# Kernel tuning notes

Measured on AMD Instinct MI355X. Metric: run time of the kernel, lower is better.

Reference implementation:

```python
import jax, jax.numpy as jnp
import numpy as np

K = 8
LN_EPS = 1e-5


def setup_inputs() -> dict:
    key = jax.random.key(0)
    ks = jax.random.split(key, 12)
    Nq, N, d = 2048, 50000, 256
    xav = np.sqrt(6.0 / (d + d)).astype(np.float32)
    inp = {
        "query": jax.random.normal(ks[0], (Nq, d), jnp.float32),
        "query_pos": jax.random.uniform(ks[1], (Nq, 3), jnp.float32) * 10.0,
        "inst_feats": jax.random.normal(ks[2], (N, d), jnp.float32),
        "sp_coords": jax.random.uniform(ks[3], (N, 3), jnp.float32) * 10.0,
        "w_q": jax.random.uniform(ks[4], (d, d), jnp.float32, -xav, xav),
        "w_v": jax.random.uniform(ks[5], (d, d), jnp.float32, -xav, xav),
        "w_o": jax.random.uniform(ks[6], (d, d), jnp.float32, -xav, xav),
        # original inits w_k/w_b to zero (uniform gate); use small random for a nontrivial gate
        "w_k": jax.random.normal(ks[7], (K, d), jnp.float32) * 0.02,
        "w_b": jax.random.normal(ks[8], (K,), jnp.float32) * 0.02,
        "gamma": jnp.ones((d,), jnp.float32),
        "beta": jnp.zeros((d,), jnp.float32),
    }
    return inp


def _knn_idx(query_pos, sp_coords, k):
    # squared euclidean distances [Nq, N] via ||q||^2 - 2 q.p + ||p||^2
    d2 = (
        jnp.sum(query_pos * query_pos, -1, keepdims=True)
        - 2.0 * (query_pos @ sp_coords.T)
        + jnp.sum(sp_coords * sp_coords, -1)[None, :]
    )
    _, idx = jax.lax.top_k(-d2, k)  # [Nq, k] nearest-neighbor indices
    return idx


def reference(query, query_pos, inst_feats, sp_coords, w_q, w_v, w_o, w_k, w_b, gamma, beta):
    idx = _knn_idx(query_pos, sp_coords, K)
    feat = inst_feats[idx]                       # [Nq, k, d] gathered neighbor feats
    q = query @ w_q.T                            # [Nq, d]
    v = feat @ w_v.T                             # [Nq, k, d]
    gate = jax.nn.softmax(q @ w_k.T + w_b, -1)   # [Nq, k]
    w = jnp.einsum("qk,qkd->qd", gate, q[:, None, :] * v)
    out = w @ w_o.T + query                      # dropout p=0 -> identity; residual
    mu = jnp.mean(out, -1, keepdims=True)
    var = jnp.mean((out - mu) ** 2, -1, keepdims=True)
    return (out - mu) * jax.lax.rsqrt(var + LN_EPS) * gamma + beta
```

## Files before the change

### kernel.cpp

```cpp
#include <hip/hip_runtime.h>
#include <math.h>

#define D        256
#define KNN      8
#define G        16
#define NCELL    (G*G*G)
#define CS       0.625f
#define EPS_D2   2e-3f
#define CAP      64
#define SPILLMAX 50000

typedef unsigned long long u64;
typedef __attribute__((ext_vector_type(8))) short bf16x8;
typedef __attribute__((ext_vector_type(4))) float f32x4;

__device__ __forceinline__ unsigned short f2b(float f) {
    unsigned u = __float_as_uint(f);
    u += 0x7fff + ((u >> 16) & 1);
    return (unsigned short)(u >> 16);
}
__device__ __forceinline__ bf16x8 pack8(float4 a, float4 b) {
    bf16x8 r;
    r[0] = (short)f2b(a.x); r[1] = (short)f2b(a.y);
    r[2] = (short)f2b(a.z); r[3] = (short)f2b(a.w);
    r[4] = (short)f2b(b.x); r[5] = (short)f2b(b.y);
    r[6] = (short)f2b(b.z); r[7] = (short)f2b(b.w);
    return r;
}

__device__ __forceinline__ unsigned enc_f32(float f) {
    unsigned b = __float_as_uint(f);
    return b ^ ((unsigned)(((int)b) >> 31) | 0x80000000u);
}
__device__ __forceinline__ float dec_f32(unsigned t) {
    unsigned m = (unsigned)(((int)t) >> 31);
    return __uint_as_float(t ^ (0x80000000u | ~m));
}
__device__ __forceinline__ u64 mkkey(float d2, int j) {
    return ((u64)enc_f32(d2) << 32) | (u64)(unsigned)j;
}
__device__ __forceinline__ int cell_of(float x) {
    int c = (int)(x * 1.6f);
    return c < 0 ? 0 : (c > G-1 ? G-1 : c);
}

__global__ __launch_bounds__(256) void prep(const float* __restrict__ w_k,
                                            const float* __restrict__ w_q,
                                            const float* __restrict__ w_v,
                                            const float* __restrict__ w_o,
                                            float* __restrict__ wk2,
                                            unsigned short* __restrict__ wqb,
                                            unsigned short* __restrict__ wvb,
                                            unsigned short* __restrict__ wob,
                                            int4* __restrict__ cnt4,
                                            int* __restrict__ spill_cnt)
{
    const int b = blockIdx.x, t = threadIdx.x;
    if (b < 8) {
        float acc = 0.f;
#pragma unroll 8
        for (int d = 0; d < D; ++d)
            acc = fmaf(w_k[b*D + d], w_q[(size_t)d*D + t], acc);
        wk2[b*D + t] = acc;
    } else if (b < 12) {
        cnt4[(b-8)*256 + t] = make_int4(0, 0, 0, 0);
        if (b == 8 && t == 0) *spill_cnt = 0;
    } else {
        const int m = (b - 12) >> 5;
        const int local = (b - 12) & 31;
        const size_t e = (size_t)local * 2048 + (size_t)t * 8;
        const float* src = (m == 0) ? w_q : (m == 1) ? w_v : w_o;
        unsigned short* dst = (m == 0) ? wqb : (m == 1) ? wvb : wob;
        const float4 x0 = *(const float4*)&src[e];
        const float4 x1 = *(const float4*)&src[e + 4];
        *(bf16x8*)&dst[e] = pack8(x0, x1);
    }
}

__global__ __launch_bounds__(256) void scatter_bins(const float* __restrict__ spc,
                                                    int* __restrict__ cnt,
                                                    float4* __restrict__ bins,
                                                    int* __restrict__ spill_cnt,
                                                    float4* __restrict__ spill, int N)
{
    const int j = blockIdx.x * 256 + threadIdx.x;
    if (j >= N) return;
    const float px = spc[3*j+0], py = spc[3*j+1], pz = spc[3*j+2];
    const int cell = cell_of(px) | (cell_of(py) << 4) | (cell_of(pz) << 8);
    const float4 p = make_float4(px, py, pz, __int_as_float(j));
    const int pos = atomicAdd(&cnt[cell], 1);
    if (pos < CAP) bins[cell*CAP + pos] = p;
    else {
        const int sp = atomicAdd(spill_cnt, 1);
        if (sp < SPILLMAX) spill[sp] = p;
    }
}

#define INSERT8(xk)                                                            \
    if ((xk) < k7) {                                                           \
        const bool c0 = (xk) < k0, c1 = (xk) < k1, c2 = (xk) < k2,             \
                   c3 = (xk) < k3, c4 = (xk) < k4, c5 = (xk) < k5,             \
                   c6 = (xk) < k6;                                             \
        k7 = c6 ? k6 : (xk);                                                   \
        k6 = c5 ? k5 : (c6 ? (xk) : k6);                                       \
        k5 = c4 ? k4 : (c5 ? (xk) : k5);                                       \
        k4 = c3 ? k3 : (c4 ? (xk) : k4);                                       \
        k3 = c2 ? k2 : (c3 ? (xk) : k3);                                       \
        k2 = c1 ? k1 : (c2 ? (xk) : k2);                                       \
        k1 = c0 ? k0 : (c1 ? (xk) : k1);                                       \
        k0 = c0 ? (xk) : k0;                                                   \
    }

#define SCORE(p)                                                               \
    {                                                                          \
        const float sp  = __fadd_rn(__fadd_rn(__fmul_rn((p).x,(p).x),          \
                                  __fmul_rn((p).y,(p).y)), __fmul_rn((p).z,(p).z)); \
        const float dot = __fmaf_rn(qz,(p).z, __fmaf_rn(qy,(p).y, __fmul_rn(qx,(p).x))); \
        const float d2  = __fadd_rn(__fsub_rn(sq, __fmul_rn(2.0f, dot)), sp);  \
        const u64 xk = mkkey(d2, __float_as_int((p).w));                       \
        INSERT8(xk)                                                            \
    }

__device__ __forceinline__ void wave_merge8(int l, u64& k0, u64& k1, u64& k2, u64& k3,
                                            u64& k4, u64& k5, u64& k6, u64& k7,
                                            u64& mine)
{
#pragma unroll
    for (int rd = 0; rd < KNN; ++rd) {
        u64 m = k0;
#pragma unroll
        for (int o = 32; o; o >>= 1) {
            const u64 t = __shfl_xor(m, o);
            if (t < m) m = t;
        }
        if (k0 == m) {
            k0 = k1; k1 = k2; k2 = k3; k3 = k4; k4 = k5; k5 = k6; k6 = k7;
            k7 = ~0ull;
        }
        if (l == rd) mine = m;
    }
}

__global__ __launch_bounds__(512) void mega2(const float* __restrict__ qpos,
                                             const float4* __restrict__ bins,
                                             const int* __restrict__ cnt,
                                             const int* __restrict__ spill_cnt,
                                             const float4* __restrict__ spill,
                                             const float* __restrict__ query,
                                             const float* __restrict__ wk2,
                                             const float* __restrict__ w_b,
                                             const float* __restrict__ feats,
                                             const unsigned short* __restrict__ wqb,
                                             const unsigned short* __restrict__ wvb,
                                             const unsigned short* __restrict__ wob,
                                             const float* __restrict__ gmm,
                                             const float* __restrict__ bta,
                                             float* __restrict__ out)
{
    __shared__ unsigned short a_lds[16][264];
    __shared__ unsigned short f_lds[16][264];
    __shared__ unsigned short w_lds[16][264];
    __shared__ float q_f32[8][260];
    __shared__ float o_f32[8][260];

    const int tid = threadIdx.x;
    const int wv  = tid >> 6, l = tid & 63;
    const int r0  = blockIdx.x * 8;

    {
        const int arr = tid >> 8;
        const int row = 8 + ((tid >> 5) & 7);
        const int o8  = (tid & 31) * 8;
        const bf16x8 z = {0,0,0,0,0,0,0,0};
        if (arr == 0) *(bf16x8*)&a_lds[row][o8] = z;
        else          *(bf16x8*)&f_lds[row][o8] = z;
    }

    {
        const int q = r0 + wv;
        const float qx = qpos[3*q+0], qy = qpos[3*q+1], qz = qpos[3*q+2];
        const float sq = __fadd_rn(__fadd_rn(__fmul_rn(qx,qx), __fmul_rn(qy,qy)),
                                   __fmul_rn(qz,qz));
        const int cx = cell_of(qx), cy = cell_of(qy), cz = cell_of(qz);

        auto bstart = [](int c, float coord) {
            const float f = coord * 1.6f - (float)c;
            int b = c + ((f < 0.5f) ? -2 : -1);
            return b < 0 ? 0 : (b > G-4 ? G-4 : b);
        };
        const int bx = bstart(cx, qx), by = bstart(cy, qy), bz = bstart(cz, qz);

        u64 k0 = ~0ull, k1 = ~0ull, k2 = ~0ull, k3 = ~0ull,
            k4 = ~0ull, k5 = ~0ull, k6 = ~0ull, k7 = ~0ull;

        {
            const int x = bx + (l & 3), y = by + ((l >> 2) & 3), z = bz + (l >> 4);
            const int ci = x | (y << 4) | (z << 8);
            const int n = min(cnt[ci], CAP);
            const int st = ci * CAP;
            for (int i = 0; i < n; ++i) { const float4 p = bins[st + i]; SCORE(p) }
        }
        {
            const int ns = min(*spill_cnt, SPILLMAX);
            for (int i = l; i < ns; i += 64) { const float4 p = spill[i]; SCORE(p) }
        }

        u64 mine = ~0ull;
        wave_merge8(l, k0, k1, k2, k3, k4, k5, k6, k7, mine);
        const u64 worst = __shfl(mine, KNN-1);

        const float w8 = dec_f32((unsigned)(worst >> 32));
        float dmin = INFINITY;
        if (bx > 0)     dmin = fminf(dmin, qx - (float)bx * CS);
        if (bx + 4 < G) dmin = fminf(dmin, (float)(bx + 4) * CS - qx);
        if (by > 0)     dmin = fminf(dmin, qy - (float)by * CS);
        if (by + 4 < G) dmin = fminf(dmin, (float)(by + 4) * CS - qy);
        if (bz > 0)     dmin = fminf(dmin, qz - (float)bz * CS);
        if (bz + 4 < G) dmin = fminf(dmin, (float)(bz + 4) * CS - qz);

        if (!(w8 + EPS_D2 <= dmin * dmin)) {
            k0 = (l < KNN) ? mine : ~0ull;
            k1 = ~0ull; k2 = ~0ull; k3 = ~0ull; k4 = ~0ull;
            k5 = ~0ull; k6 = ~0ull; k7 = ~0ull;
            for (int c = l; c < NCELL; c += 64) {
                const int x = c & 15, y = (c >> 4) & 15, z = c >> 8;
                if (x >= bx && x < bx+4 && y >= by && y < by+4 && z >= bz && z < bz+4) continue;
                const int n = min(cnt[c], CAP);
                const int st = c * CAP;
                for (int i = 0; i < n; ++i) { const float4 p = bins[st + i]; SCORE(p) }
            }
            wave_merge8(l, k0, k1, k2, k3, k4, k5, k6, k7, mine);
        }

        int ids[KNN];
        const int my_id = (int)(unsigned)(mine & 0xffffffffu);
#pragma unroll
        for (int j = 0; j < KNN; ++j) ids[j] = __shfl(my_id, j);

        const float4 qv = *(const float4*)&query[(size_t)q*D + l*4];
        float logit[KNN];
#pragma unroll
        for (int j = 0; j < KNN; ++j) {
            const float4 w = *(const float4*)&wk2[(size_t)j*D + l*4];
            logit[j] = fmaf(qv.x, w.x, fmaf(qv.y, w.y, fmaf(qv.z, w.z, qv.w*w.w)));
        }
#pragma unroll
        for (int o = 32; o; o >>= 1) {
#pragma unroll
            for (int j = 0; j < KNN; ++j) logit[j] += __shfl_xor(logit[j], o);
        }
#pragma unroll
        for (int j = 0; j < KNN; ++j) logit[j] += w_b[j];

        float m = logit[0];
#pragma unroll
        for (int j = 1; j < KNN; ++j) m = fmaxf(m, logit[j]);
        float e[KNN]; float ssum = 0.f;
#pragma unroll
        for (int j = 0; j < KNN; ++j) { e[j] = expf(logit[j] - m); ssum += e[j]; }
        const float inv = 1.f / ssum;

        float4 acc4 = make_float4(0.f, 0.f, 0.f, 0.f);
#pragma unroll
        for (int j = 0; j < KNN; ++j) {
            const float gj = e[j] * inv;
            const float4 f = *(const float4*)&feats[(size_t)ids[j]*D + l*4];
            acc4.x = fmaf(gj, f.x, acc4.x);
            acc4.y = fmaf(gj, f.y, acc4.y);
            acc4.z = fmaf(gj, f.z, acc4.z);
            acc4.w = fmaf(gj, f.w, acc4.w);
        }

        *(float4*)&q_f32[wv][l*4] = qv;
        short4 qb; qb.x = (short)f2b(qv.x); qb.y = (short)f2b(qv.y);
                   qb.z = (short)f2b(qv.z); qb.w = (short)f2b(qv.w);
        *(short4*)&a_lds[wv][l*4] = qb;
        short4 fb; fb.x = (short)f2b(acc4.x); fb.y = (short)f2b(acc4.y);
                   fb.z = (short)f2b(acc4.z); fb.w = (short)f2b(acc4.w);
        *(short4*)&f_lds[wv][l*4] = fb;
    }
    __syncthreads();

    const int mrow = l & 15;
    const int kq   = (l >> 4) * 8;

    f32x4 aq[2], av[2];
#pragma unroll
    for (int t = 0; t < 2; ++t) {
        aq[t] = (f32x4){0.f, 0.f, 0.f, 0.f};
        av[t] = (f32x4){0.f, 0.f, 0.f, 0.f};
    }
#pragma unroll
    for (int k0 = 0; k0 < D; k0 += 32) {
        const bf16x8 af = *(const bf16x8*)&a_lds[mrow][k0 + kq];
        const bf16x8 ff = *(const bf16x8*)&f_lds[mrow][k0 + kq];
#pragma unroll
        for (int t = 0; t < 2; ++t) {
            const int n = wv*32 + t*16 + mrow;
            const bf16x8 bq = *(const bf16x8*)&wqb[(size_t)n*D + k0 + kq];
            const bf16x8 bv = *(const bf16x8*)&wvb[(size_t)n*D + k0 + kq];
            aq[t] = __builtin_amdgcn_mfma_f32_16x16x32_bf16(af, bq, aq[t], 0, 0, 0);
            av[t] = __builtin_amdgcn_mfma_f32_16x16x32_bf16(ff, bv, av[t], 0, 0, 0);
        }
    }

#pragma unroll
    for (int t = 0; t < 2; ++t) {
#pragma unroll
        for (int r = 0; r < 4; ++r) {
            const int row = (l >> 4) * 4 + r;
            const int col = wv*32 + t*16 + (l & 15);
            w_lds[row][col] = f2b(aq[t][r] * av[t][r]);
        }
    }
    __syncthreads();

    f32x4 ao[2];
#pragma unroll
    for (int t = 0; t < 2; ++t) ao[t] = (f32x4){0.f, 0.f, 0.f, 0.f};
#pragma unroll
    for (int k0 = 0; k0 < D; k0 += 32) {
        const bf16x8 wf = *(const bf16x8*)&w_lds[mrow][k0 + kq];
#pragma unroll
        for (int t = 0; t < 2; ++t) {
            const int n = wv*32 + t*16 + mrow;
            const bf16x8 bo = *(const bf16x8*)&wob[(size_t)n*D + k0 + kq];
            ao[t] = __builtin_amdgcn_mfma_f32_16x16x32_bf16(wf, bo, ao[t], 0, 0, 0);
        }
    }
#pragma unroll
    for (int t = 0; t < 2; ++t) {
#pragma unroll
        for (int r = 0; r < 4; ++r) {
            const int row = (l >> 4) * 4 + r;
            if (row < 8) {
                const int col = wv*32 + t*16 + (l & 15);
                o_f32[row][col] = ao[t][r] + q_f32[row][col];
            }
        }
    }
    __syncthreads();

    {
        const float4 v = *(const float4*)&o_f32[wv][l*4];
        float s  = (v.x + v.y) + (v.z + v.w);
        float s2 = fmaf(v.x, v.x, fmaf(v.y, v.y, fmaf(v.z, v.z, v.w*v.w)));
#pragma unroll
        for (int o = 32; o; o >>= 1) { s += __shfl_xor(s, o); s2 += __shfl_xor(s2, o); }
        const float mu  = s * (1.f/256.f);
        const float var = fmaf(s2, 1.f/256.f, -mu*mu);
        const float rs  = rsqrtf(var + 1e-5f);
        const float4 g = *(const float4*)&gmm[l*4];
        const float4 b = *(const float4*)&bta[l*4];
        float4 o4;
        o4.x = (v.x - mu) * rs * g.x + b.x;
        o4.y = (v.y - mu) * rs * g.y + b.y;
        o4.z = (v.z - mu) * rs * g.z + b.z;
        o4.w = (v.w - mu) * rs * g.w + b.w;
        *(float4*)&out[(size_t)(r0+wv)*D + l*4] = o4;
    }
}

extern "C" void kernel_launch(void* const* d_in, const int* in_sizes, int n_in,
                              void* d_out, int out_size, void* d_ws, size_t ws_size,
                              hipStream_t stream)
{
    const float* query = (const float*)d_in[0];
    const float* qpos  = (const float*)d_in[1];
    const float* feats = (const float*)d_in[2];
    const float* spc   = (const float*)d_in[3];
    const float* w_q   = (const float*)d_in[4];
    const float* w_v   = (const float*)d_in[5];
    const float* w_o   = (const float*)d_in[6];
    const float* w_k   = (const float*)d_in[7];
    const float* w_b   = (const float*)d_in[8];
    const float* gamma = (const float*)d_in[9];
    const float* beta  = (const float*)d_in[10];

    const int Nq = in_sizes[0] / D;
    const int N  = in_sizes[2] / D;

    char* ws = (char*)d_ws;
    size_t off = 0;
    int* cnt = (int*)(ws + off);               off += ((size_t)NCELL * 4 + 255) & ~(size_t)255;
    int* spill_cnt = (int*)(ws + off);         off += 256;
    float* wk2 = (float*)(ws + off);           off += ((size_t)KNN * D * 4 + 255) & ~(size_t)255;
    unsigned short* wqb = (unsigned short*)(ws + off); off += (size_t)D * D * 2;
    unsigned short* wvb = (unsigned short*)(ws + off); off += (size_t)D * D * 2;
    unsigned short* wob = (unsigned short*)(ws + off); off += (size_t)D * D * 2;
    float4* bins = (float4*)(ws + off);        off += ((size_t)NCELL * CAP * 16 + 255) & ~(size_t)255;
    float4* spill = (float4*)(ws + off);       off += ((size_t)SPILLMAX * 16 + 255) & ~(size_t)255;

    prep<<<108, 256, 0, stream>>>(w_k, w_q, w_v, w_o, wk2, wqb, wvb, wob,
                                  (int4*)cnt, spill_cnt);
    scatter_bins<<<(N + 255)/256, 256, 0, stream>>>(spc, cnt, bins, spill_cnt, spill, N);
    mega2<<<Nq/8, 512, 0, stream>>>(qpos, bins, cnt, spill_cnt, spill,
                                    query, wk2, w_b, feats, wqb, wvb, wob,
                                    gamma, beta, (float*)d_out);
}
```

Baseline: 52.81 us.

## Fuse prep, binning and attention into one cooperative persistent kernel

Replaces the three launches (weight prep, spatial binning scatter, main kNN+MLP kernel) with a single cooperative kernel of 512 blocks that uses grid-wide syncs between phases, then loops persistently over 4-query tiles. The per-block tile shrinks from 8 to 4 queries with 256 threads, each wave covering 64 output columns. This removes kernel launch gaps at the cost of grid.sync overhead and a persistent loop that reloads the weight fragments per tile. The old three-kernel path remains as a fallback if the cooperative launch fails.

```diff
diff --git a/kernel.cpp b/kernel.cpp
--- a/kernel.cpp
+++ b/kernel.cpp
@@ -1,5 +1,8 @@
 #include <hip/hip_runtime.h>
+#include <hip/hip_cooperative_groups.h>
 #include <math.h>
+
+namespace cg = cooperative_groups;
 
 #define D        256
 #define KNN      8
@@ -9,6 +12,7 @@
 #define EPS_D2   2e-3f
 #define CAP      64
 #define SPILLMAX 50000
+#define GRIDC    512
 
 typedef unsigned long long u64;
 typedef __attribute__((ext_vector_type(8))) short bf16x8;
@@ -42,6 +46,332 @@
 __device__ __forceinline__ int cell_of(float x) {
     int c = (int)(x * 1.6f);
     return c < 0 ? 0 : (c > G-1 ? G-1 : c);
+}
+
+#define INSERT8(xk)                                                            \
+    if ((xk) < k7) {                                                           \
+        const bool c0 = (xk) < k0, c1 = (xk) < k1, c2 = (xk) < k2,             \
+                   c3 = (xk) < k3, c4 = (xk) < k4, c5 = (xk) < k5,             \
+                   c6 = (xk) < k6;                                             \
+        k7 = c6 ? k6 : (xk);                                                   \
+        k6 = c5 ? k5 : (c6 ? (xk) : k6);                                       \
+        k5 = c4 ? k4 : (c5 ? (xk) : k5);                                       \
+        k4 = c3 ? k3 : (c4 ? (xk) : k4);                                       \
+        k3 = c2 ? k2 : (c3 ? (xk) : k3);                                       \
+        k2 = c1 ? k1 : (c2 ? (xk) : k2);                                       \
+        k1 = c0 ? k0 : (c1 ? (xk) : k1);                                       \
+        k0 = c0 ? (xk) : k0;                                                   \
+    }
+
+#define SCORE(p)                                                               \
+    {                                                                          \
+        const float sp  = __fadd_rn(__fadd_rn(__fmul_rn((p).x,(p).x),          \
+                                  __fmul_rn((p).y,(p).y)), __fmul_rn((p).z,(p).z)); \
+        const float dot = __fmaf_rn(qz,(p).z, __fmaf_rn(qy,(p).y, __fmul_rn(qx,(p).x))); \
+        const float d2  = __fadd_rn(__fsub_rn(sq, __fmul_rn(2.0f, dot)), sp);  \
+        const u64 xk = mkkey(d2, __float_as_int((p).w));                       \
+        INSERT8(xk)                                                            \
+    }
+
+__device__ __forceinline__ void wave_merge8(int l, u64& k0, u64& k1, u64& k2, u64& k3,
+                                            u64& k4, u64& k5, u64& k6, u64& k7,
+                                            u64& mine)
+{
+#pragma unroll
+    for (int rd = 0; rd < KNN; ++rd) {
+        u64 m = k0;
+#pragma unroll
+        for (int o = 32; o; o >>= 1) {
+            const u64 t = __shfl_xor(m, o);
+            if (t < m) m = t;
+        }
+        if (k0 == m) {
+            k0 = k1; k1 = k2; k2 = k3; k3 = k4; k4 = k5; k5 = k6; k6 = k7;
+            k7 = ~0ull;
+        }
+        if (l == rd) mine = m;
+    }
+}
+
+__device__ __forceinline__ void knn_gate_wave(int q, int l,
+                                              const float* __restrict__ qpos,
+                                              const float4* __restrict__ bins,
+                                              const int* __restrict__ cnt,
+                                              const int* __restrict__ spill_cnt,
+                                              const float4* __restrict__ spill,
+                                              const float* __restrict__ query,
+                                              const float* __restrict__ wk2,
+                                              const float* __restrict__ w_b,
+                                              const float* __restrict__ feats,
+                                              float4& qv_out, float4& fb_out)
+{
+    const float qx = qpos[3*q+0], qy = qpos[3*q+1], qz = qpos[3*q+2];
+    const float sq = __fadd_rn(__fadd_rn(__fmul_rn(qx,qx), __fmul_rn(qy,qy)),
+                               __fmul_rn(qz,qz));
+    const int cx = cell_of(qx), cy = cell_of(qy), cz = cell_of(qz);
+
+    auto bstart = [](int c, float coord) {
+        const float f = coord * 1.6f - (float)c;
+        int b = c + ((f < 0.5f) ? -2 : -1);
+        return b < 0 ? 0 : (b > G-4 ? G-4 : b);
+    };
+    const int bx = bstart(cx, qx), by = bstart(cy, qy), bz = bstart(cz, qz);
+
+    u64 k0 = ~0ull, k1 = ~0ull, k2 = ~0ull, k3 = ~0ull,
+        k4 = ~0ull, k5 = ~0ull, k6 = ~0ull, k7 = ~0ull;
+
+    {
+        const int x = bx + (l & 3), y = by + ((l >> 2) & 3), z = bz + (l >> 4);
+        const int ci = x | (y << 4) | (z << 8);
+        const int n = min(cnt[ci], CAP);
+        const int st = ci * CAP;
+        for (int i = 0; i < n; ++i) { const float4 p = bins[st + i]; SCORE(p) }
+    }
+    {
+        const int ns = min(*spill_cnt, SPILLMAX);
+        for (int i = l; i < ns; i += 64) { const float4 p = spill[i]; SCORE(p) }
+    }
+
+    u64 mine = ~0ull;
+    wave_merge8(l, k0, k1, k2, k3, k4, k5, k6, k7, mine);
+    const u64 worst = __shfl(mine, KNN-1);
+
+    const float w8 = dec_f32((unsigned)(worst >> 32));
+    float dmin = INFINITY;
+    if (bx > 0)     dmin = fminf(dmin, qx - (float)bx * CS);
+    if (bx + 4 < G) dmin = fminf(dmin, (float)(bx + 4) * CS - qx);
+    if (by > 0)     dmin = fminf(dmin, qy - (float)by * CS);
+    if (by + 4 < G) dmin = fminf(dmin, (float)(by + 4) * CS - qy);
+    if (bz > 0)     dmin = fminf(dmin, qz - (float)bz * CS);
+    if (bz + 4 < G) dmin = fminf(dmin, (float)(bz + 4) * CS - qz);
+
+    if (!(w8 + EPS_D2 <= dmin * dmin)) {
+        k0 = (l < KNN) ? mine : ~0ull;
+        k1 = ~0ull; k2 = ~0ull; k3 = ~0ull; k4 = ~0ull;
+        k5 = ~0ull; k6 = ~0ull; k7 = ~0ull;
+        for (int c = l; c < NCELL; c += 64) {
+            const int x = c & 15, y = (c >> 4) & 15, z = c >> 8;
+            if (x >= bx && x < bx+4 && y >= by && y < by+4 && z >= bz && z < bz+4) continue;
+            const int n = min(cnt[c], CAP);
+            const int st = c * CAP;
+            for (int i = 0; i < n; ++i) { const float4 p = bins[st + i]; SCORE(p) }
+        }
+        wave_merge8(l, k0, k1, k2, k3, k4, k5, k6, k7, mine);
+    }
+
+    int ids[KNN];
+    const int my_id = (int)(unsigned)(mine & 0xffffffffu);
+#pragma unroll
+    for (int j = 0; j < KNN; ++j) ids[j] = __shfl(my_id, j);
+
+    const float4 qv = *(const float4*)&query[(size_t)q*D + l*4];
+    float logit[KNN];
+#pragma unroll
+    for (int j = 0; j < KNN; ++j) {
+        const float4 w = *(const float4*)&wk2[(size_t)j*D + l*4];
+        logit[j] = fmaf(qv.x, w.x, fmaf(qv.y, w.y, fmaf(qv.z, w.z, qv.w*w.w)));
+    }
+#pragma unroll
+    for (int o = 32; o; o >>= 1) {
+#pragma unroll
+        for (int j = 0; j < KNN; ++j) logit[j] += __shfl_xor(logit[j], o);
+    }
+#pragma unroll
+    for (int j = 0; j < KNN; ++j) logit[j] += w_b[j];
+
+    float m = logit[0];
+#pragma unroll
+    for (int j = 1; j < KNN; ++j) m = fmaxf(m, logit[j]);
+    float e[KNN]; float ssum = 0.f;
+#pragma unroll
+    for (int j = 0; j < KNN; ++j) { e[j] = expf(logit[j] - m); ssum += e[j]; }
+    const float inv = 1.f / ssum;
+
+    float4 acc4 = make_float4(0.f, 0.f, 0.f, 0.f);
+#pragma unroll
+    for (int j = 0; j < KNN; ++j) {
+        const float gj = e[j] * inv;
+        const float4 f = *(const float4*)&feats[(size_t)ids[j]*D + l*4];
+        acc4.x = fmaf(gj, f.x, acc4.x);
+        acc4.y = fmaf(gj, f.y, acc4.y);
+        acc4.z = fmaf(gj, f.z, acc4.z);
+        acc4.w = fmaf(gj, f.w, acc4.w);
+    }
+    qv_out = qv;
+    fb_out = acc4;
+}
+
+struct MegaParams {
+    const float* qpos; const float* spc; const float* query; const float* feats;
+    const float* w_k; const float* w_q; const float* w_v; const float* w_o;
+    const float* w_b; const float* gmm; const float* bta;
+    float* wk2;
+    unsigned short* wqb; unsigned short* wvb; unsigned short* wob;
+    int* cnt; int* spill_cnt; float4* bins; float4* spill;
+    float* out;
+    int N; int Nq;
+};
+
+__global__ __launch_bounds__(256, 2) void megacoop(MegaParams P)
+{
+    __shared__ unsigned short a_lds[16][264];
+    __shared__ unsigned short f_lds[16][264];
+    __shared__ unsigned short w_lds[16][264];
+    __shared__ float q_f32[4][260];
+    __shared__ float o_f32[4][260];
+
+    cg::grid_group gg = cg::this_grid();
+    const int tid = threadIdx.x;
+    const int g   = blockIdx.x * 256 + tid;
+    const int wv  = tid >> 6, l = tid & 63;
+
+    if (g < 16384) {
+        const int o = g >> 3, sub = g & 7;
+        const int row = o >> 8, col = o & 255;
+        float acc = 0.f;
+#pragma unroll 8
+        for (int i = 0; i < 32; ++i) {
+            const int d = sub * 32 + i;
+            acc = fmaf(P.w_k[row*D + d], P.w_q[(size_t)d*D + col], acc);
+        }
+        acc += __shfl_xor(acc, 1);
+        acc += __shfl_xor(acc, 2);
+        acc += __shfl_xor(acc, 4);
+        if (sub == 0) P.wk2[o] = acc;
+    } else if (g < 17408) {
+        ((int4*)P.cnt)[g - 16384] = make_int4(0, 0, 0, 0);
+        if (g == 16384) *P.spill_cnt = 0;
+    } else if (g < 41984) {
+        const int o = g - 17408;
+        const int m = o >> 13, local = o & 8191;
+        const size_t e = (size_t)local * 8;
+        const float* src = (m == 0) ? P.w_q : (m == 1) ? P.w_v : P.w_o;
+        unsigned short* dst = (m == 0) ? P.wqb : (m == 1) ? P.wvb : P.wob;
+        const float4 x0 = *(const float4*)&src[e];
+        const float4 x1 = *(const float4*)&src[e + 4];
+        *(bf16x8*)&dst[e] = pack8(x0, x1);
+    }
+    gg.sync();
+
+    if (g < P.N) {
+        const int j = g;
+        const float px = P.spc[3*j+0], py = P.spc[3*j+1], pz = P.spc[3*j+2];
+        const int cell = cell_of(px) | (cell_of(py) << 4) | (cell_of(pz) << 8);
+        const float4 p = make_float4(px, py, pz, __int_as_float(j));
+        const int pos = atomicAdd(&P.cnt[cell], 1);
+        if (pos < CAP) P.bins[cell*CAP + pos] = p;
+        else {
+            const int sp = atomicAdd(P.spill_cnt, 1);
+            if (sp < SPILLMAX) P.spill[sp] = p;
+        }
+    }
+    gg.sync();
+
+    for (int t0 = blockIdx.x * 4; t0 < P.Nq; t0 += GRIDC * 4) {
+#pragma unroll
+        for (int k = 0; k < 3; ++k) {
+            const int o = tid + k * 256;
+            const int oo = (o < 384) ? o : o - 384;
+            const int row = 4 + (oo >> 5);
+            const int c8 = (oo & 31) * 8;
+            const bf16x8 z = {0,0,0,0,0,0,0,0};
+            if (o < 384) *(bf16x8*)&a_lds[row][c8] = z;
+            else         *(bf16x8*)&f_lds[row][c8] = z;
+        }
+
+        {
+            float4 qv, fb;
+            knn_gate_wave(t0 + wv, l, P.qpos, P.bins, P.cnt, P.spill_cnt, P.spill,
+                          P.query, P.wk2, P.w_b, P.feats, qv, fb);
+            *(float4*)&q_f32[wv][l*4] = qv;
+            short4 qb; qb.x = (short)f2b(qv.x); qb.y = (short)f2b(qv.y);
+                       qb.z = (short)f2b(qv.z); qb.w = (short)f2b(qv.w);
+            *(short4*)&a_lds[wv][l*4] = qb;
+            short4 fv; fv.x = (short)f2b(fb.x); fv.y = (short)f2b(fb.y);
+                       fv.z = (short)f2b(fb.z); fv.w = (short)f2b(fb.w);
+            *(short4*)&f_lds[wv][l*4] = fv;
+        }
+        __syncthreads();
+
+        const int mrow = l & 15;
+        const int kq   = (l >> 4) * 8;
+
+        f32x4 aq[4], av[4];
+#pragma unroll
+        for (int t = 0; t < 4; ++t) {
+            aq[t] = (f32x4){0.f, 0.f, 0.f, 0.f};
+            av[t] = (f32x4){0.f, 0.f, 0.f, 0.f};
+        }
+#pragma unroll
+        for (int k0 = 0; k0 < D; k0 += 32) {
+            const bf16x8 af = *(const bf16x8*)&a_lds[mrow][k0 + kq];
+            const bf16x8 ff = *(const bf16x8*)&f_lds[mrow][k0 + kq];
+#pragma unroll
+            for (int t = 0; t < 4; ++t) {
+                const int n = wv*64 + t*16 + mrow;
+                const bf16x8 bq = *(const bf16x8*)&P.wqb[(size_t)n*D + k0 + kq];
+                const bf16x8 bv = *(const bf16x8*)&P.wvb[(size_t)n*D + k0 + kq];
+                aq[t] = __builtin_amdgcn_mfma_f32_16x16x32_bf16(af, bq, aq[t], 0, 0, 0);
+                av[t] = __builtin_amdgcn_mfma_f32_16x16x32_bf16(ff, bv, av[t], 0, 0, 0);
+            }
+        }
+#pragma unroll
+        for (int t = 0; t < 4; ++t) {
+#pragma unroll
+            for (int r = 0; r < 4; ++r) {
+                const int row = (l >> 4) * 4 + r;
+                const int col = wv*64 + t*16 + (l & 15);
+                w_lds[row][col] = f2b(aq[t][r] * av[t][r]);
+            }
+        }
+        __syncthreads();
+
+        f32x4 ao[4];
+#pragma unroll
+        for (int t = 0; t < 4; ++t) ao[t] = (f32x4){0.f, 0.f, 0.f, 0.f};
+#pragma unroll
+        for (int k0 = 0; k0 < D; k0 += 32) {
+            const bf16x8 wf = *(const bf16x8*)&w_lds[mrow][k0 + kq];
+#pragma unroll
+            for (int t = 0; t < 4; ++t) {
+                const int n = wv*64 + t*16 + mrow;
+                const bf16x8 bo = *(const bf16x8*)&P.wob[(size_t)n*D + k0 + kq];
+                ao[t] = __builtin_amdgcn_mfma_f32_16x16x32_bf16(wf, bo, ao[t], 0, 0, 0);
+            }
+        }
+#pragma unroll
+        for (int t = 0; t < 4; ++t) {
+#pragma unroll
+            for (int r = 0; r < 4; ++r) {
+                const int row = (l >> 4) * 4 + r;
+                if (row < 4) {
+                    const int col = wv*64 + t*16 + (l & 15);
+                    o_f32[row][col] = ao[t][r] + q_f32[row][col];
+                }
+            }
+        }
+        __syncthreads();
+
+        {
+            const float4 v = *(const float4*)&o_f32[wv][l*4];
+            float s  = (v.x + v.y) + (v.z + v.w);
+            float s2 = fmaf(v.x, v.x, fmaf(v.y, v.y, fmaf(v.z, v.z, v.w*v.w)));
+#pragma unroll
+            for (int o = 32; o; o >>= 1) { s += __shfl_xor(s, o); s2 += __shfl_xor(s2, o); }
+            const float mu  = s * (1.f/256.f);
+            const float var = fmaf(s2, 1.f/256.f, -mu*mu);
+            const float rs  = rsqrtf(var + 1e-5f);
+            const float4 gm = *(const float4*)&P.gmm[l*4];
+            const float4 bt = *(const float4*)&P.bta[l*4];
+            float4 o4;
+            o4.x = (v.x - mu) * rs * gm.x + bt.x;
+            o4.y = (v.y - mu) * rs * gm.y + bt.y;
+            o4.z = (v.z - mu) * rs * gm.z + bt.z;
+            o4.w = (v.w - mu) * rs * gm.w + bt.w;
+            *(float4*)&P.out[(size_t)(t0+wv)*D + l*4] = o4;
+        }
+        __syncthreads();
+    }
 }
 
 __global__ __launch_bounds__(256) void prep(const float* __restrict__ w_k,
@@ -96,51 +426,6 @@
     }
 }
 
-#define INSERT8(xk)                                                            \
-    if ((xk) < k7) {                                                           \
-        const bool c0 = (xk) < k0, c1 = (xk) < k1, c2 = (xk) < k2,             \
-                   c3 = (xk) < k3, c4 = (xk) < k4, c5 = (xk) < k5,             \
-                   c6 = (xk) < k6;                                             \
-        k7 = c6 ? k6 : (xk);                                                   \
-        k6 = c5 ? k5 : (c6 ? (xk) : k6);                                       \
-        k5 = c4 ? k4 : (c5 ? (xk) : k5);                                       \
-        k4 = c3 ? k3 : (c4 ? (xk) : k4);                                       \
-        k3 = c2 ? k2 : (c3 ? (xk) : k3);                                       \
-        k2 = c1 ? k1 : (c2 ? (xk) : k2);                                       \
-        k1 = c0 ? k0 : (c1 ? (xk) : k1);                                       \
-        k0 = c0 ? (xk) : k0;                                                   \
-    }
-
-#define SCORE(p)                                                               \
-    {                                                                          \
-        const float sp  = __fadd_rn(__fadd_rn(__fmul_rn((p).x,(p).x),          \
-                                  __fmul_rn((p).y,(p).y)), __fmul_rn((p).z,(p).z)); \
-        const float dot = __fmaf_rn(qz,(p).z, __fmaf_rn(qy,(p).y, __fmul_rn(qx,(p).x))); \
-        const float d2  = __fadd_rn(__fsub_rn(sq, __fmul_rn(2.0f, dot)), sp);  \
-        const u64 xk = mkkey(d2, __float_as_int((p).w));                       \
-        INSERT8(xk)                                                            \
-    }
-
-__device__ __forceinline__ void wave_merge8(int l, u64& k0, u64& k1, u64& k2, u64& k3,
-                                            u64& k4, u64& k5, u64& k6, u64& k7,
-                                            u64& mine)
-{
-#pragma unroll
-    for (int rd = 0; rd < KNN; ++rd) {
-        u64 m = k0;
-#pragma unroll
-        for (int o = 32; o; o >>= 1) {
-            const u64 t = __shfl_xor(m, o);
-            if (t < m) m = t;
-        }
-        if (k0 == m) {
-            k0 = k1; k1 = k2; k2 = k3; k3 = k4; k4 = k5; k5 = k6; k6 = k7;
-            k7 = ~0ull;
-        }
-        if (l == rd) mine = m;
-    }
-}
-
 __global__ __launch_bounds__(512) void mega2(const float* __restrict__ qpos,
                                              const float4* __restrict__ bins,
                                              const int* __restrict__ cnt,
@@ -177,107 +462,16 @@
     }
 
     {
-        const int q = r0 + wv;
-        const float qx = qpos[3*q+0], qy = qpos[3*q+1], qz = qpos[3*q+2];
-        const float sq = __fadd_rn(__fadd_rn(__fmul_rn(qx,qx), __fmul_rn(qy,qy)),
-                                   __fmul_rn(qz,qz));
-        const int cx = cell_of(qx), cy = cell_of(qy), cz = cell_of(qz);
-
-        auto bstart = [](int c, float coord) {
-            const float f = coord * 1.6f - (float)c;
-            int b = c + ((f < 0.5f) ? -2 : -1);
-            return b < 0 ? 0 : (b > G-4 ? G-4 : b);
-        };
-        const int bx = bstart(cx, qx), by = bstart(cy, qy), bz = bstart(cz, qz);
-
-        u64 k0 = ~0ull, k1 = ~0ull, k2 = ~0ull, k3 = ~0ull,
-            k4 = ~0ull, k5 = ~0ull, k6 = ~0ull, k7 = ~0ull;
-
-        {
-            const int x = bx + (l & 3), y = by + ((l >> 2) & 3), z = bz + (l >> 4);
-            const int ci = x | (y << 4) | (z << 8);
-            const int n = min(cnt[ci], CAP);
-            const int st = ci * CAP;
-            for (int i = 0; i < n; ++i) { const float4 p = bins[st + i]; SCORE(p) }
-        }
-        {
-            const int ns = min(*spill_cnt, SPILLMAX);
-            for (int i = l; i < ns; i += 64) { const float4 p = spill[i]; SCORE(p) }
-        }
-
-        u64 mine = ~0ull;
-        wave_merge8(l, k0, k1, k2, k3, k4, k5, k6, k7, mine);
-        const u64 worst = __shfl(mine, KNN-1);
-
-        const float w8 = dec_f32((unsigned)(worst >> 32));
-        float dmin = INFINITY;
-        if (bx > 0)     dmin = fminf(dmin, qx - (float)bx * CS);
-        if (bx + 4 < G) dmin = fminf(dmin, (float)(bx + 4) * CS - qx);
-        if (by > 0)     dmin = fminf(dmin, qy - (float)by * CS);
-        if (by + 4 < G) dmin = fminf(dmin, (float)(by + 4) * CS - qy);
-        if (bz > 0)     dmin = fminf(dmin, qz - (float)bz * CS);
-        if (bz + 4 < G) dmin = fminf(dmin, (float)(bz + 4) * CS - qz);
-
-        if (!(w8 + EPS_D2 <= dmin * dmin)) {
-            k0 = (l < KNN) ? mine : ~0ull;
-            k1 = ~0ull; k2 = ~0ull; k3 = ~0ull; k4 = ~0ull;
-            k5 = ~0ull; k6 = ~0ull; k7 = ~0ull;
-            for (int c = l; c < NCELL; c += 64) {
-                const int x = c & 15, y = (c >> 4) & 15, z = c >> 8;
-                if (x >= bx && x < bx+4 && y >= by && y < by+4 && z >= bz && z < bz+4) continue;
-                const int n = min(cnt[c], CAP);
-                const int st = c * CAP;
-                for (int i = 0; i < n; ++i) { const float4 p = bins[st + i]; SCORE(p) }
-            }
-            wave_merge8(l, k0, k1, k2, k3, k4, k5, k6, k7, mine);
-        }
-
-        int ids[KNN];
-        const int my_id = (int)(unsigned)(mine & 0xffffffffu);
-#pragma unroll
-        for (int j = 0; j < KNN; ++j) ids[j] = __shfl(my_id, j);
-
-        const float4 qv = *(const float4*)&query[(size_t)q*D + l*4];
-        float logit[KNN];
-#pragma unroll
-        for (int j = 0; j < KNN; ++j) {
-            const float4 w = *(const float4*)&wk2[(size_t)j*D + l*4];
-            logit[j] = fmaf(qv.x, w.x, fmaf(qv.y, w.y, fmaf(qv.z, w.z, qv.w*w.w)));
-        }
-#pragma unroll
-        for (int o = 32; o; o >>= 1) {
-#pragma unroll
-            for (int j = 0; j < KNN; ++j) logit[j] += __shfl_xor(logit[j], o);
-        }
-#pragma unroll
-        for (int j = 0; j < KNN; ++j) logit[j] += w_b[j];
-
-        float m = logit[0];
-#pragma unroll
-        for (int j = 1; j < KNN; ++j) m = fmaxf(m, logit[j]);
-        float e[KNN]; float ssum = 0.f;
-#pragma unroll
-        for (int j = 0; j < KNN; ++j) { e[j] = expf(logit[j] - m); ssum += e[j]; }
-        const float inv = 1.f / ssum;
-
-        float4 acc4 = make_float4(0.f, 0.f, 0.f, 0.f);
-#pragma unroll
-        for (int j = 0; j < KNN; ++j) {
-            const float gj = e[j] * inv;
-            const float4 f = *(const float4*)&feats[(size_t)ids[j]*D + l*4];
-            acc4.x = fmaf(gj, f.x, acc4.x);
-            acc4.y = fmaf(gj, f.y, acc4.y);
-            acc4.z = fmaf(gj, f.z, acc4.z);
-            acc4.w = fmaf(gj, f.w, acc4.w);
-        }
-
+        float4 qv, fb;
+        knn_gate_wave(r0 + wv, l, qpos, bins, cnt, spill_cnt, spill,
+                      query, wk2, w_b, feats, qv, fb);
         *(float4*)&q_f32[wv][l*4] = qv;
         short4 qb; qb.x = (short)f2b(qv.x); qb.y = (short)f2b(qv.y);
                    qb.z = (short)f2b(qv.z); qb.w = (short)f2b(qv.w);
         *(short4*)&a_lds[wv][l*4] = qb;
-        short4 fb; fb.x = (short)f2b(acc4.x); fb.y = (short)f2b(acc4.y);
-                   fb.z = (short)f2b(acc4.z); fb.w = (short)f2b(acc4.w);
-        *(short4*)&f_lds[wv][l*4] = fb;
+        short4 fv; fv.x = (short)f2b(fb.x); fv.y = (short)f2b(fb.y);
+                   fv.z = (short)f2b(fb.z); fv.w = (short)f2b(fb.w);
+        *(short4*)&f_lds[wv][l*4] = fv;
     }
     __syncthreads();
 
@@ -303,7 +497,6 @@
             av[t] = __builtin_amdgcn_mfma_f32_16x16x32_bf16(ff, bv, av[t], 0, 0, 0);
         }
     }
-
 #pragma unroll
     for (int t = 0; t < 2; ++t) {
 #pragma unroll
@@ -365,36 +558,43 @@
                               void* d_out, int out_size, void* d_ws, size_t ws_size,
                               hipStream_t stream)
 {
-    const float* query = (const float*)d_in[0];
-    const float* qpos  = (const float*)d_in[1];
-    const float* feats = (const float*)d_in[2];
-    const float* spc   = (const float*)d_in[3];
-    const float* w_q   = (const float*)d_in[4];
-    const float* w_v   = (const float*)d_in[5];
-    const float* w_o   = (const float*)d_in[6];
-    const float* w_k   = (const float*)d_in[7];
-    const float* w_b   = (const float*)d_in[8];
-    const float* gamma = (const float*)d_in[9];
-    const float* beta  = (const float*)d_in[10];
-
-    const int Nq = in_sizes[0] / D;
-    const int N  = in_sizes[2] / D;
+    MegaParams P;
+    P.query = (const float*)d_in[0];
+    P.qpos  = (const float*)d_in[1];
+    P.feats = (const float*)d_in[2];
+    P.spc   = (const float*)d_in[3];
+    P.w_q   = (const float*)d_in[4];
+    P.w_v   = (const float*)d_in[5];
+    P.w_o   = (const float*)d_in[6];
+    P.w_k   = (const float*)d_in[7];
+    P.w_b   = (const float*)d_in[8];
+    P.gmm   = (const float*)d_in[9];
+    P.bta   = (const float*)d_in[10];
+    P.Nq = in_sizes[0] / D;
+    P.N  = in_sizes[2] / D;
+    P.out = (float*)d_out;
 
     char* ws = (char*)d_ws;
     size_t off = 0;
-    int* cnt = (int*)(ws + off);               off += ((size_t)NCELL * 4 + 255) & ~(size_t)255;
-    int* spill_cnt = (int*)(ws + off);         off += 256;
-    float* wk2 = (float*)(ws + off);           off += ((size_t)KNN * D * 4 + 255) & ~(size_t)255;
-    unsigned short* wqb = (unsigned short*)(ws + off); off += (size_t)D * D * 2;
-    unsigned short* wvb = (unsigned short*)(ws + off); off += (size_t)D * D * 2;
-    unsigned short* wob = (unsigned short*)(ws + off); off += (size_t)D * D * 2;
-    float4* bins = (float4*)(ws + off);        off += ((size_t)NCELL * CAP * 16 + 255) & ~(size_t)255;
-    float4* spill = (float4*)(ws + off);       off += ((size_t)SPILLMAX * 16 + 255) & ~(size_t)255;
-
-    prep<<<108, 256, 0, stream>>>(w_k, w_q, w_v, w_o, wk2, wqb, wvb, wob,
-                                  (int4*)cnt, spill_cnt);
-    scatter_bins<<<(N + 255)/256, 256, 0, stream>>>(spc, cnt, bins, spill_cnt, spill, N);
-    mega2<<<Nq/8, 512, 0, stream>>>(qpos, bins, cnt, spill_cnt, spill,
-                                    query, wk2, w_b, feats, wqb, wvb, wob,
-                                    gamma, beta, (float*)d_out);
-}
+    P.cnt = (int*)(ws + off);               off += ((size_t)NCELL * 4 + 255) & ~(size_t)255;
+    P.spill_cnt = (int*)(ws + off);         off += 256;
+    P.wk2 = (float*)(ws + off);             off += ((size_t)KNN * D * 4 + 255) & ~(size_t)255;
+    P.wqb = (unsigned short*)(ws + off);    off += (size_t)D * D * 2;
+    P.wvb = (unsigned short*)(ws + off);    off += (size_t)D * D * 2;
+    P.wob = (unsigned short*)(ws + off);    off += (size_t)D * D * 2;
+    P.bins = (float4*)(ws + off);           off += ((size_t)NCELL * CAP * 16 + 255) & ~(size_t)255;
+    P.spill = (float4*)(ws + off);          off += ((size_t)SPILLMAX * 16 + 255) & ~(size_t)255;
+
+    void* args[] = { (void*)&P };
+    hipError_t e = hipLaunchCooperativeKernel((const void*)megacoop, dim3(GRIDC),
+                                              dim3(256), args, 0, stream);
+    if (e != hipSuccess) {
+        prep<<<108, 256, 0, stream>>>(P.w_k, P.w_q, P.w_v, P.w_o, P.wk2,
+                                      P.wqb, P.wvb, P.wob, (int4*)P.cnt, P.spill_cnt);
+        scatter_bins<<<(P.N + 255)/256, 256, 0, stream>>>(P.spc, P.cnt, P.bins,
+                                                          P.spill_cnt, P.spill, P.N);
+        mega2<<<P.Nq/8, 512, 0, stream>>>(P.qpos, P.bins, P.cnt, P.spill_cnt, P.spill,
+                                          P.query, P.wk2, P.w_b, P.feats,
+                                          P.wqb, P.wvb, P.wob, P.gmm, P.bta, P.out);
+    }
+}
```

Result: slower. 176.9 us (+235.0%).
